# Kernel optimization log

Hardware: AMD Instinct MI355X
Metric: run time of the kernel (lower is better)

Reference implementation:

```python
import jax, jax.numpy as jnp
import numpy as np

FEATURES = 768

def setup_inputs() -> dict:
    key = jax.random.key(0)
    k1, k2, kq, kd, kc = jax.random.split(key, 5)
    B, S1, S2 = 8, 2048, 2048
    bound = 1.0 / np.sqrt(FEATURES)  # nn.Linear default init range
    return {
        "matrix1": jax.random.normal(k1, (B, S1, FEATURES), dtype=jnp.float32),
        "matrix2": jax.random.normal(k2, (B, S2, FEATURES), dtype=jnp.float32),
        "w_q": jax.random.uniform(kq, (FEATURES,), jnp.float32, -bound, bound),
        "w_d": jax.random.uniform(kd, (FEATURES,), jnp.float32, -bound, bound),
        "w_c": jax.random.uniform(kc, (FEATURES,), jnp.float32, -bound, bound),
    }

def reference(matrix1, matrix2, w_q, w_d, w_c):
    # S[b,j,k] = (m1 @ w_q)[b,j] + (m2 @ w_d)[b,k] + sum_f w_c[f]*m1[b,j,f]*m2[b,k,f]
    Q = jnp.einsum('bjf,f->bj', matrix1, w_q)                # [B, S1]
    D = jnp.einsum('bkf,f->bk', matrix2, w_d)                # [B, S2]
    C = jnp.einsum('bjf,bkf->bjk', matrix1 * w_c, matrix2)   # [B, S1, S2]
    return Q[:, :, None] + D[:, None, :] + C
```

## Files before the change

kernel.cpp:

```cpp
#include <hip/hip_runtime.h>
#include <hip/hip_bf16.h>

#define S1 2048
#define S2 2048
#define FEAT 768
#define NB 8
#define BM 256
#define BN 256
#define BK 32
#define NKT (FEAT / BK)
#define KTILE_BYTES 32768
#define NBUF 4

typedef __attribute__((ext_vector_type(8))) short bf16x8;
typedef __attribute__((ext_vector_type(4))) float f32x4;
typedef __attribute__((ext_vector_type(4))) unsigned short us4;
typedef __attribute__((address_space(1))) const unsigned int gu32;
typedef __attribute__((address_space(3))) unsigned int lu32;

static __device__ __forceinline__ unsigned short f2bf(float x) {
    unsigned u = __builtin_bit_cast(unsigned, x);
    unsigned r = u + 0x7FFFu + ((u >> 16) & 1u);
    return (unsigned short)(r >> 16);
}

__global__ __launch_bounds__(256) void conv_kernel(
    const float* __restrict__ m1, const float* __restrict__ m2,
    const float* __restrict__ wq, const float* __restrict__ wd,
    const float* __restrict__ wc,
    unsigned short* __restrict__ A, unsigned short* __restrict__ Bm,
    float* __restrict__ Q, float* __restrict__ D) {
    int wave = threadIdx.x >> 6;
    int lane = threadIdx.x & 63;
    int g = blockIdx.x * 4 + wave;
    bool isA = (g < NB * S1);
    int row = isA ? g : g - NB * S1;
    const float* src = isA ? m1 : m2;
    const float* w   = isA ? wq : wd;
    unsigned short* dst = (isA ? A : Bm) + (size_t)row * FEAT;
    const float4* rp = (const float4*)(src + (size_t)row * FEAT);
    const float4* wp = (const float4*)w;
    const float4* cp = (const float4*)wc;
    float acc = 0.f;
#pragma unroll
    for (int i = 0; i < 3; ++i) {
        int idx = lane + 64 * i;
        float4 a = rp[idx];
        float4 b = wp[idx];
        acc += a.x * b.x + a.y * b.y + a.z * b.z + a.w * b.w;
        float4 c;
        if (isA) c = cp[idx]; else c = float4{1.f, 1.f, 1.f, 1.f};
        us4 v = { f2bf(a.x * c.x), f2bf(a.y * c.y),
                  f2bf(a.z * c.z), f2bf(a.w * c.w) };
        *(us4*)(dst + idx * 4) = v;
    }
#pragma unroll
    for (int s = 32; s; s >>= 1) acc += __shfl_xor(acc, s, 64);
    if (lane == 0) (isA ? Q : D)[row] = acc;
}

#define STAGE(kt) do {                                                            \
    const int _buf = (kt) & (NBUF - 1);                                           \
    const char* _As = Ab + (kt) * (BK * 2);                                       \
    const char* _Bs = Bb + (kt) * (BK * 2);                                       \
    char* _lA = ldsb + _buf * KTILE_BYTES;                                        \
    char* _lB = _lA + 16384;                                                      \
    _Pragma("unroll")                                                             \
    for (int _r = 0; _r < 2; ++_r) {                                              \
        const int _rowb = _r * 128 + wave * 16;                                   \
        __builtin_amdgcn_global_load_lds(                                         \
            (gu32*)(_As + (size_t)(_rowb + srow) * (FEAT * 2) + scol),            \
            (lu32*)(_lA + _rowb * 64), 16, 0, 0);                                 \
        __builtin_amdgcn_global_load_lds(                                         \
            (gu32*)(_Bs + (size_t)(_rowb + srow) * (FEAT * 2) + scol),            \
            (lu32*)(_lB + _rowb * 64), 16, 0, 0);                                 \
    }                                                                             \
} while (0)

__global__ __launch_bounds__(512, 2) void gemm256_kernel(
    const unsigned short* __restrict__ A, const unsigned short* __restrict__ Bm,
    const float* __restrict__ Q, const float* __restrict__ D,
    float* __restrict__ out) {

    extern __shared__ __align__(16) char ldsb[];

    const int bid = blockIdx.x;
    const int swz = (bid & 7) * 64 + (bid >> 3);
    const int b  = swz >> 6;
    const int t  = swz & 63;
    const int tm = t >> 3, tn = t & 7;

    const int tid  = threadIdx.x;
    const int lane = tid & 63;
    const int wave = tid >> 6;
    const int wm = wave >> 2, wn = wave & 3;

    const char* Ab = (const char*)(A + ((size_t)b * S1 + (size_t)tm * BM) * FEAT);
    const char* Bb = (const char*)(Bm + ((size_t)b * S2 + (size_t)tn * BN) * FEAT);

    const int srow = lane >> 2;
    const int scol = (lane & 3) * 16;

    const int fr   = lane & 15;
    const int fkg  = (lane >> 4) * 16;

    f32x4 acc[8][4];
#pragma unroll
    for (int m = 0; m < 8; ++m)
#pragma unroll
        for (int n = 0; n < 4; ++n) acc[m][n] = (f32x4)0.f;

    STAGE(0);
    STAGE(1);
    asm volatile("s_waitcnt vmcnt(4)" ::: "memory");
    __builtin_amdgcn_s_barrier();
    asm volatile("" ::: "memory");

#pragma unroll 4
    for (int kt = 0; kt < NKT; ++kt) {
        if (kt + 2 < NKT) STAGE(kt + 2);

        const char* lA = ldsb + (kt & (NBUF - 1)) * KTILE_BYTES;
        const char* lB = lA + 16384;

        bf16x8 bfr[4], af[8];
#pragma unroll
        for (int n = 0; n < 4; ++n)
            bfr[n] = *(const bf16x8*)(lB + (wn * 64 + n * 16 + fr) * 64 + fkg);
#pragma unroll
        for (int m = 0; m < 8; ++m)
            af[m] = *(const bf16x8*)(lA + (wm * 128 + m * 16 + fr) * 64 + fkg);

        __builtin_amdgcn_s_setprio(1);
#pragma unroll
        for (int m = 0; m < 8; ++m)
#pragma unroll
            for (int n = 0; n < 4; ++n)
                acc[m][n] = __builtin_amdgcn_mfma_f32_16x16x32_bf16(
                    af[m], bfr[n], acc[m][n], 0, 0, 0);
        __builtin_amdgcn_s_setprio(0);

        if (kt + 1 < NKT) {
            if (kt + 2 < NKT) asm volatile("s_waitcnt vmcnt(4)" ::: "memory");
            else              asm volatile("s_waitcnt vmcnt(0)" ::: "memory");
            __builtin_amdgcn_s_barrier();
            asm volatile("" ::: "memory");
        }
    }

    const float* Qb = Q + b * S1 + tm * BM;
    const float* Db = D + b * S2 + tn * BN;
    float dv[4];
#pragma unroll
    for (int n = 0; n < 4; ++n) dv[n] = Db[wn * 64 + n * 16 + fr];

    const size_t outbase = ((size_t)b * S1 + (size_t)tm * BM) * S2 + (size_t)tn * BN;
#pragma unroll
    for (int m = 0; m < 8; ++m) {
#pragma unroll
        for (int i = 0; i < 4; ++i) {
            int rl = wm * 128 + m * 16 + (lane >> 4) * 4 + i;
            float qv = Qb[rl];
            float* orow = out + outbase + (size_t)rl * S2 + wn * 64;
#pragma unroll
            for (int n = 0; n < 4; ++n)
                orow[n * 16 + fr] = acc[m][n][i] + qv + dv[n];
        }
    }
}

__global__ __launch_bounds__(256) void qd_kernel(
    const float* __restrict__ m1, const float* __restrict__ m2,
    const float* __restrict__ wq, const float* __restrict__ wd,
    float* __restrict__ Q, float* __restrict__ D) {
    int wave = threadIdx.x >> 6;
    int lane = threadIdx.x & 63;
    int g = blockIdx.x * 4 + wave;
    const float* src; const float* w; float* dst; int row;
    if (g < NB * S1) { src = m1; w = wq; dst = Q; row = g; }
    else             { src = m2; w = wd; dst = D; row = g - NB * S1; }
    const float4* rp = (const float4*)(src + (size_t)row * FEAT);
    const float4* wp = (const float4*)w;
    float acc = 0.f;
#pragma unroll
    for (int i = 0; i < 3; ++i) {
        float4 a = rp[lane + 64 * i];
        float4 b = wp[lane + 64 * i];
        acc += a.x * b.x + a.y * b.y + a.z * b.z + a.w * b.w;
    }
#pragma unroll
    for (int s = 32; s; s >>= 1) acc += __shfl_xor(acc, s, 64);
    if (lane == 0) dst[row] = acc;
}

__global__ __launch_bounds__(256) void gemm_kernel(
    const float* __restrict__ m1, const float* __restrict__ m2,
    const float* __restrict__ wc,
    const float* __restrict__ Q, const float* __restrict__ D,
    float* __restrict__ out) {

    __shared__ __align__(16) char sA[128 * 64 * 2];
    __shared__ __align__(16) char sB[128 * 64 * 2];
    __shared__ float wcs[FEAT];

    const int tid = threadIdx.x;
    const int blk = blockIdx.x;
    const int b  = blk >> 8;
    const int t  = blk & 255;
    const int tm = t >> 4, tn = t & 15;

    for (int i = tid; i < FEAT; i += 256) wcs[i] = wc[i];

    const float* Abase = m1 + ((size_t)b * S1 + (size_t)tm * 128) * FEAT;
    const float* Bbase = m2 + ((size_t)b * S2 + (size_t)tn * 128) * FEAT;

    const int lane = tid & 63;
    const int wave = tid >> 6;
    const int wm = wave >> 1, wn = wave & 1;

    f32x4 acc[4][4];
#pragma unroll
    for (int m = 0; m < 4; ++m)
#pragma unroll
        for (int n = 0; n < 4; ++n) acc[m][n] = (f32x4)0.f;

    const int col4 = tid & 15;
    const int row0 = tid >> 4;

    __syncthreads();

    for (int ks = 0; ks < FEAT / 64; ++ks) {
        float4 wc4 = *(const float4*)&wcs[ks * 64 + col4 * 4];
        const float4* Ak = (const float4*)(Abase + ks * 64);
        const float4* Bk = (const float4*)(Bbase + ks * 64);

        __syncthreads();
#pragma unroll
        for (int i = 0; i < 8; ++i) {
            int r = row0 + 16 * i;
            float4 a = Ak[(size_t)r * (FEAT / 4) + col4];
            us4 av = { f2bf(a.x * wc4.x), f2bf(a.y * wc4.y),
                       f2bf(a.z * wc4.z), f2bf(a.w * wc4.w) };
            int off = r * 128 + ((col4 * 8) ^ ((r & 7) << 4));
            *(us4*)(sA + off) = av;
        }
#pragma unroll
        for (int i = 0; i < 8; ++i) {
            int r = row0 + 16 * i;
            float4 v = Bk[(size_t)r * (FEAT / 4) + col4];
            us4 bv = { f2bf(v.x), f2bf(v.y), f2bf(v.z), f2bf(v.w) };
            int off = r * 128 + ((col4 * 8) ^ ((r & 7) << 4));
            *(us4*)(sB + off) = bv;
        }
        __syncthreads();

#pragma unroll
        for (int s = 0; s < 2; ++s) {
            bf16x8 af[4], bfr[4];
#pragma unroll
            for (int m = 0; m < 4; ++m) {
                int r = wm * 64 + m * 16 + (lane & 15);
                int coff = (s * 64 + (lane >> 4) * 16) ^ ((r & 7) << 4);
                af[m] = *(const bf16x8*)(sA + r * 128 + coff);
            }
#pragma unroll
            for (int n = 0; n < 4; ++n) {
                int r = wn * 64 + n * 16 + (lane & 15);
                int coff = (s * 64 + (lane >> 4) * 16) ^ ((r & 7) << 4);
                bfr[n] = *(const bf16x8*)(sB + r * 128 + coff);
            }
#pragma unroll
            for (int m = 0; m < 4; ++m)
#pragma unroll
                for (int n = 0; n < 4; ++n)
                    acc[m][n] = __builtin_amdgcn_mfma_f32_16x16x32_bf16(
                        af[m], bfr[n], acc[m][n], 0, 0, 0);
        }
    }

    const float* Qb = Q + b * S1 + tm * 128;
    const float* Db = D + b * S2 + tn * 128;
    float dv[4];
#pragma unroll
    for (int n = 0; n < 4; ++n) dv[n] = Db[wn * 64 + n * 16 + (lane & 15)];

    const size_t outbase = ((size_t)b * S1 + (size_t)tm * 128) * S2 + (size_t)tn * 128;
#pragma unroll
    for (int m = 0; m < 4; ++m) {
#pragma unroll
        for (int i = 0; i < 4; ++i) {
            int rl = wm * 64 + m * 16 + (lane >> 4) * 4 + i;
            float qv = Qb[rl];
            float* orow = out + outbase + (size_t)rl * S2 + wn * 64;
#pragma unroll
            for (int n = 0; n < 4; ++n) {
                int cl = n * 16 + (lane & 15);
                orow[cl] = acc[m][n][i] + qv + dv[n];
            }
        }
    }
}

extern "C" void kernel_launch(void* const* d_in, const int* in_sizes, int n_in,
                              void* d_out, int out_size, void* d_ws, size_t ws_size,
                              hipStream_t stream) {
    const float* m1 = (const float*)d_in[0];
    const float* m2 = (const float*)d_in[1];
    const float* wq = (const float*)d_in[2];
    const float* wd = (const float*)d_in[3];
    const float* wc = (const float*)d_in[4];
    float* out = (float*)d_out;

    const size_t elems = (size_t)NB * S1 * FEAT;
    const size_t need = 2 * elems * sizeof(unsigned short)
                      + (size_t)(NB * S1 + NB * S2) * sizeof(float);

    if (ws_size >= need) {
        unsigned short* Abuf = (unsigned short*)d_ws;
        unsigned short* Bbuf = Abuf + elems;
        float* Q  = (float*)(Bbuf + elems);
        float* Dv = Q + NB * S1;
        conv_kernel<<<(NB * S1 + NB * S2) / 4, 256, 0, stream>>>(
            m1, m2, wq, wd, wc, Abuf, Bbuf, Q, Dv);
        gemm256_kernel<<<NB * (S1 / BM) * (S2 / BN), 512, NBUF * KTILE_BYTES, stream>>>(
            Abuf, Bbuf, Q, Dv, out);
    } else {
        float* Q  = (float*)d_ws;
        float* Dv = Q + NB * S1;
        qd_kernel<<<(2 * NB * S1) / 4, 256, 0, stream>>>(m1, m2, wq, wd, Q, Dv);
        gemm_kernel<<<NB * 256, 256, 0, stream>>>(m1, m2, wc, Q, Dv, out);
    }
}
```

Baseline: 95.30 us.

## Swizzle LDS tiles, double-buffer MFMA fragments, and deepen global prefetch

Fragments for the next K-tile are now read from LDS into a second register set while the MFMAs for the current tile run. Global-to-LDS prefetch goes one tile deeper, using three of the four LDS buffers in flight. The global source column is XOR-swizzled by row, and the matching LDS read applies the same swizzle, to cut LDS bank conflicts on fragment loads. The second fragment set adds about 48 VGPRs under a 512-thread, 2-block launch bound, so register spills or lower occupancy are a risk.

```diff
diff --git a/kernel.cpp b/kernel.cpp
--- a/kernel.cpp
+++ b/kernel.cpp
@@ -69,12 +69,23 @@
     for (int _r = 0; _r < 2; ++_r) {                                              \
         const int _rowb = _r * 128 + wave * 16;                                   \
         __builtin_amdgcn_global_load_lds(                                         \
-            (gu32*)(_As + (size_t)(_rowb + srow) * (FEAT * 2) + scol),            \
+            (gu32*)(_As + (size_t)(_rowb + srow) * (FEAT * 2) + scolsw),          \
             (lu32*)(_lA + _rowb * 64), 16, 0, 0);                                 \
         __builtin_amdgcn_global_load_lds(                                         \
-            (gu32*)(_Bs + (size_t)(_rowb + srow) * (FEAT * 2) + scol),            \
+            (gu32*)(_Bs + (size_t)(_rowb + srow) * (FEAT * 2) + scolsw),          \
             (lu32*)(_lB + _rowb * 64), 16, 0, 0);                                 \
     }                                                                             \
+} while (0)
+
+#define LOADFRAGS(set, ktidx) do {                                                \
+    const char* _lA = ldsb + ((ktidx) & (NBUF - 1)) * KTILE_BYTES;                \
+    const char* _lB = _lA + 16384;                                                \
+    _Pragma("unroll")                                                             \
+    for (int _n = 0; _n < 4; ++_n)                                                \
+        bfx[set][_n] = *(const bf16x8*)(_lB + (wn * 64 + _n * 16 + fr) * 64 + fkb);\
+    _Pragma("unroll")                                                             \
+    for (int _m = 0; _m < 8; ++_m)                                                \
+        afr[set][_m] = *(const bf16x8*)(_lA + (wm * 128 + _m * 16 + fr) * 64 + fkb);\
 } while (0)
 
 __global__ __launch_bounds__(512, 2) void gemm256_kernel(
@@ -98,38 +109,34 @@
     const char* Ab = (const char*)(A + ((size_t)b * S1 + (size_t)tm * BM) * FEAT);
     const char* Bb = (const char*)(Bm + ((size_t)b * S2 + (size_t)tn * BN) * FEAT);
 
-    const int srow = lane >> 2;
-    const int scol = (lane & 3) * 16;
-
-    const int fr   = lane & 15;
-    const int fkg  = (lane >> 4) * 16;
+    const int srow   = lane >> 2;
+    const int scolsw = (((lane & 3) ^ ((lane >> 3) & 3)) * 16);
+
+    const int fr  = lane & 15;
+    const int fkb = (((lane >> 4) ^ ((lane >> 1) & 3)) * 16);
 
     f32x4 acc[8][4];
 #pragma unroll
     for (int m = 0; m < 8; ++m)
 #pragma unroll
         for (int n = 0; n < 4; ++n) acc[m][n] = (f32x4)0.f;
+
+    bf16x8 afr[2][8];
+    bf16x8 bfx[2][4];
 
     STAGE(0);
     STAGE(1);
+    STAGE(2);
     asm volatile("s_waitcnt vmcnt(4)" ::: "memory");
     __builtin_amdgcn_s_barrier();
     asm volatile("" ::: "memory");
-
-#pragma unroll 4
+    LOADFRAGS(0, 0);
+
+#pragma unroll 2
     for (int kt = 0; kt < NKT; ++kt) {
-        if (kt + 2 < NKT) STAGE(kt + 2);
-
-        const char* lA = ldsb + (kt & (NBUF - 1)) * KTILE_BYTES;
-        const char* lB = lA + 16384;
-
-        bf16x8 bfr[4], af[8];
-#pragma unroll
-        for (int n = 0; n < 4; ++n)
-            bfr[n] = *(const bf16x8*)(lB + (wn * 64 + n * 16 + fr) * 64 + fkg);
-#pragma unroll
-        for (int m = 0; m < 8; ++m)
-            af[m] = *(const bf16x8*)(lA + (wm * 128 + m * 16 + fr) * 64 + fkg);
+        const int cur = kt & 1, nxt = cur ^ 1;
+        if (kt + 3 < NKT) STAGE(kt + 3);
+        if (kt + 1 < NKT) LOADFRAGS(nxt, kt + 1);
 
         __builtin_amdgcn_s_setprio(1);
 #pragma unroll
@@ -137,11 +144,11 @@
 #pragma unroll
             for (int n = 0; n < 4; ++n)
                 acc[m][n] = __builtin_amdgcn_mfma_f32_16x16x32_bf16(
-                    af[m], bfr[n], acc[m][n], 0, 0, 0);
+                    afr[cur][m], bfx[cur][n], acc[m][n], 0, 0, 0);
         __builtin_amdgcn_s_setprio(0);
 
         if (kt + 1 < NKT) {
-            if (kt + 2 < NKT) asm volatile("s_waitcnt vmcnt(4)" ::: "memory");
+            if (kt + 3 < NKT) asm volatile("s_waitcnt vmcnt(4)" ::: "memory");
             else              asm volatile("s_waitcnt vmcnt(0)" ::: "memory");
             __builtin_amdgcn_s_barrier();
             asm volatile("" ::: "memory");
```

After: 93.29 us. -2.1%, faster.

## Rework GEMM into 8-phase pipeline with BK=64, XOR-swizzled LDS, double buffering

Applied to the files above, without the earlier changes.

Replaces the 4-buffer BK=32 GEMM main loop with a BK=64 double-buffered scheme. Each k-tile is split into four 16KB quarter-loads issued one per phase, interleaved with eight compute phases per two k-tiles. LDS rows are XOR-swizzled to avoid bank conflicts on the wider 128-byte rows. Launch bounds drop to one block per CU because 128KB of LDS is used, which trades occupancy for finer-grained overlap and adds two barriers per phase.

```diff
diff --git a/kernel.cpp b/kernel.cpp
--- a/kernel.cpp
+++ b/kernel.cpp
@@ -7,10 +7,11 @@
 #define NB 8
 #define BM 256
 #define BN 256
-#define BK 32
+#define BK 64
 #define NKT (FEAT / BK)
-#define KTILE_BYTES 32768
-#define NBUF 4
+#define ITERS (NKT / 2)
+#define HALF_BYTES 16384
+#define KT_BYTES   65536
 
 typedef __attribute__((ext_vector_type(8))) short bf16x8;
 typedef __attribute__((ext_vector_type(4))) float f32x4;
@@ -59,25 +60,21 @@
     if (lane == 0) (isA ? Q : D)[row] = acc;
 }
 
-#define STAGE(kt) do {                                                            \
-    const int _buf = (kt) & (NBUF - 1);                                           \
-    const char* _As = Ab + (kt) * (BK * 2);                                       \
-    const char* _Bs = Bb + (kt) * (BK * 2);                                       \
-    char* _lA = ldsb + _buf * KTILE_BYTES;                                        \
-    char* _lB = _lA + 16384;                                                      \
+#define STAGE_H(_kts, _half) do {                                                 \
+    const char* _s = ((_half) < 2 ? Ab : Bb);                                     \
+    const int _ro = ((_half) & 1) * 128;                                          \
+    char* _d = ldsb + ((_kts) & 1) * KT_BYTES + (_half) * HALF_BYTES;             \
     _Pragma("unroll")                                                             \
-    for (int _r = 0; _r < 2; ++_r) {                                              \
-        const int _rowb = _r * 128 + wave * 16;                                   \
+    for (int _i = 0; _i < 2; ++_i) {                                              \
+        const int _rb = _i * 64 + wave * 8;                                       \
         __builtin_amdgcn_global_load_lds(                                         \
-            (gu32*)(_As + (size_t)(_rowb + srow) * (FEAT * 2) + scol),            \
-            (lu32*)(_lA + _rowb * 64), 16, 0, 0);                                 \
-        __builtin_amdgcn_global_load_lds(                                         \
-            (gu32*)(_Bs + (size_t)(_rowb + srow) * (FEAT * 2) + scol),            \
-            (lu32*)(_lB + _rowb * 64), 16, 0, 0);                                 \
+            (gu32*)(_s + (size_t)(_ro + _rb + srow8) * (FEAT * 2)                 \
+                       + (_kts) * (BK * 2) + scol8),                              \
+            (lu32*)(_d + _rb * 128), 16, 0, 0);                                   \
     }                                                                             \
 } while (0)
 
-__global__ __launch_bounds__(512, 2) void gemm256_kernel(
+__global__ __launch_bounds__(512, 1) void gemm8p_kernel(
     const unsigned short* __restrict__ A, const unsigned short* __restrict__ Bm,
     const float* __restrict__ Q, const float* __restrict__ D,
     float* __restrict__ out) {
@@ -87,8 +84,8 @@
     const int bid = blockIdx.x;
     const int swz = (bid & 7) * 64 + (bid >> 3);
     const int b  = swz >> 6;
-    const int t  = swz & 63;
-    const int tm = t >> 3, tn = t & 7;
+    const int t0 = swz & 63;
+    const int tm = t0 >> 3, tn = t0 & 7;
 
     const int tid  = threadIdx.x;
     const int lane = tid & 63;
@@ -98,11 +95,12 @@
     const char* Ab = (const char*)(A + ((size_t)b * S1 + (size_t)tm * BM) * FEAT);
     const char* Bb = (const char*)(Bm + ((size_t)b * S2 + (size_t)tn * BN) * FEAT);
 
-    const int srow = lane >> 2;
-    const int scol = (lane & 3) * 16;
-
-    const int fr   = lane & 15;
-    const int fkg  = (lane >> 4) * 16;
+    const int srow8 = lane >> 3;
+    const int scol8 = ((lane & 7) ^ (srow8 & 7)) * 16;
+
+    const int fr  = lane & 15;
+    const int kg  = lane >> 4;
+    const int frbase = fr * 128 + ((kg ^ (fr & 7)) << 4);
 
     f32x4 acc[8][4];
 #pragma unroll
@@ -110,39 +108,82 @@
 #pragma unroll
         for (int n = 0; n < 4; ++n) acc[m][n] = (f32x4)0.f;
 
-    STAGE(0);
-    STAGE(1);
-    asm volatile("s_waitcnt vmcnt(4)" ::: "memory");
+    bf16x8 aR0[4], aR1[4];
+    bf16x8 bR0[4], bR1[4];
+
+    STAGE_H(0, 0); STAGE_H(0, 1); STAGE_H(0, 2); STAGE_H(0, 3);
+    STAGE_H(1, 0);
+    asm volatile("s_waitcnt vmcnt(2)" ::: "memory");
     __builtin_amdgcn_s_barrier();
     asm volatile("" ::: "memory");
 
-#pragma unroll 4
-    for (int kt = 0; kt < NKT; ++kt) {
-        if (kt + 2 < NKT) STAGE(kt + 2);
-
-        const char* lA = ldsb + (kt & (NBUF - 1)) * KTILE_BYTES;
-        const char* lB = lA + 16384;
-
-        bf16x8 bfr[4], af[8];
-#pragma unroll
-        for (int n = 0; n < 4; ++n)
-            bfr[n] = *(const bf16x8*)(lB + (wn * 64 + n * 16 + fr) * 64 + fkg);
-#pragma unroll
-        for (int m = 0; m < 8; ++m)
-            af[m] = *(const bf16x8*)(lA + (wm * 128 + m * 16 + fr) * 64 + fkg);
-
-        __builtin_amdgcn_s_setprio(1);
-#pragma unroll
-        for (int m = 0; m < 8; ++m)
-#pragma unroll
-            for (int n = 0; n < 4; ++n)
-                acc[m][n] = __builtin_amdgcn_mfma_f32_16x16x32_bf16(
-                    af[m], bfr[n], acc[m][n], 0, 0, 0);
-        __builtin_amdgcn_s_setprio(0);
-
-        if (kt + 1 < NKT) {
-            if (kt + 2 < NKT) asm volatile("s_waitcnt vmcnt(4)" ::: "memory");
-            else              asm volatile("s_waitcnt vmcnt(0)" ::: "memory");
+    for (int t = 0; t < ITERS; ++t) {
+#pragma unroll
+        for (int p = 0; p < 8; ++p) {
+            const int ktc = 2 * t + (p >> 2);
+            const char* buf = ldsb + (size_t)(ktc & 1) * KT_BYTES;
+            const char* lA = buf + wm * HALF_BYTES;
+            const char* lB = buf + 2 * HALF_BYTES + (wn >> 1) * HALF_BYTES
+                                 + (wn & 1) * 8192;
+            const int q  = p & 3;
+            const int mh = q >> 1, nh = q & 1;
+
+            if (q == 0) {
+#pragma unroll
+                for (int mm = 0; mm < 4; ++mm) {
+                    aR0[mm] = *(const bf16x8*)(lA + mm * 2048 + frbase);
+                    aR1[mm] = *(const bf16x8*)(lA + mm * 2048 + (frbase ^ 64));
+                }
+#pragma unroll
+                for (int nn = 0; nn < 2; ++nn) {
+                    bR0[nn] = *(const bf16x8*)(lB + nn * 2048 + frbase);
+                    bR1[nn] = *(const bf16x8*)(lB + nn * 2048 + (frbase ^ 64));
+                }
+            } else if (q == 1) {
+#pragma unroll
+                for (int nn = 2; nn < 4; ++nn) {
+                    bR0[nn] = *(const bf16x8*)(lB + nn * 2048 + frbase);
+                    bR1[nn] = *(const bf16x8*)(lB + nn * 2048 + (frbase ^ 64));
+                }
+            } else if (q == 2) {
+#pragma unroll
+                for (int mm = 0; mm < 4; ++mm) {
+                    aR0[mm] = *(const bf16x8*)(lA + 8192 + mm * 2048 + frbase);
+                    aR1[mm] = *(const bf16x8*)(lA + 8192 + mm * 2048 + (frbase ^ 64));
+                }
+            }
+
+            {
+                const int kts  = 2 * t + ((p + 5) >> 2);
+                const int half = (p + 5) & 3;
+                if (kts < NKT) STAGE_H(kts, half);
+            }
+
+            asm volatile("" ::: "memory");
+            __builtin_amdgcn_s_barrier();
+            asm volatile("" ::: "memory");
+
+            __builtin_amdgcn_s_setprio(1);
+#pragma unroll
+            for (int mm = 0; mm < 4; ++mm)
+#pragma unroll
+                for (int nn = 0; nn < 2; ++nn) {
+                    const int mg = mh * 4 + mm, ng = nh * 2 + nn;
+                    acc[mg][ng] = __builtin_amdgcn_mfma_f32_16x16x32_bf16(
+                        aR0[mm], bR0[ng], acc[mg][ng], 0, 0, 0);
+                    acc[mg][ng] = __builtin_amdgcn_mfma_f32_16x16x32_bf16(
+                        aR1[mm], bR1[ng], acc[mg][ng], 0, 0, 0);
+                }
+            __builtin_amdgcn_s_setprio(0);
+
+            if (p == 3) {
+                if (t == ITERS - 1) asm volatile("s_waitcnt vmcnt(0)" ::: "memory");
+                else                asm volatile("s_waitcnt vmcnt(2)" ::: "memory");
+            }
+            if (p == 7 && t < ITERS - 1)
+                asm volatile("s_waitcnt vmcnt(2)" ::: "memory");
+
+            asm volatile("" ::: "memory");
             __builtin_amdgcn_s_barrier();
             asm volatile("" ::: "memory");
         }
@@ -159,7 +200,7 @@
     for (int m = 0; m < 8; ++m) {
 #pragma unroll
         for (int i = 0; i < 4; ++i) {
-            int rl = wm * 128 + m * 16 + (lane >> 4) * 4 + i;
+            int rl = wm * 128 + m * 16 + kg * 4 + i;
             float qv = Qb[rl];
             float* orow = out + outbase + (size_t)rl * S2 + wn * 64;
 #pragma unroll
@@ -322,7 +363,7 @@
         float* Dv = Q + NB * S1;
         conv_kernel<<<(NB * S1 + NB * S2) / 4, 256, 0, stream>>>(
             m1, m2, wq, wd, wc, Abuf, Bbuf, Q, Dv);
-        gemm256_kernel<<<NB * (S1 / BM) * (S2 / BN), 512, NBUF * KTILE_BYTES, stream>>>(
+        gemm8p_kernel<<<NB * (S1 / BM) * (S2 / BN), 512, 2 * KT_BYTES, stream>>>(
             Abuf, Bbuf, Q, Dv, out);
     } else {
         float* Q  = (float*)d_ws;
```

Result: no change. 95.66 us (+0.4%).
